# Kernel optimization log

Measured on AMD Instinct MI355X. Metric: run time of the kernel, lower is better.

The kernel has to match this reference:

```python
import jax, jax.numpy as jnp
import numpy as np


def setup_inputs() -> dict:
    key = jax.random.key(0)
    k1, k2, k3, k4 = jax.random.split(key, 4)
    B, N, F_in, F_out = 8, 2048, 256, 256
    v = jax.random.normal(k1, (B, N, F_in), dtype=jnp.float32)
    adj = jax.random.uniform(k2, (B, N, N), dtype=jnp.float32)  # pairwise distances
    # torch Linear weights: [out_features, in_features], scaled like kaiming-uniform-ish
    W1 = jax.random.normal(k3, (F_out, F_in), dtype=jnp.float32) * (1.0 / np.sqrt(F_in))
    W2 = jax.random.normal(k4, (F_out, F_in), dtype=jnp.float32) * (1.0 / np.sqrt(F_in))
    return {"v": v, "adj": adj, "W1": W1, "W2": W2}


def reference(v, adj, W1, W2):
    D = 100.0
    # Linear projections (no bias): [B,N,F_in] @ [F_in,F_out]
    c1 = jnp.einsum("bnf,of->bno", v, W1)
    c2 = jnp.einsum("bnf,of->bno", v, W2)
    # Pairwise scores: [B,N,N]
    s = jnp.einsum("bno,bmo->bnm", c1, c2)
    c = jax.nn.sigmoid(s) * D + 1e-05
    c = 1.0 / (2.0 * c * c)
    norm_adj = jnp.exp(-(adj * adj * c))
    return (v, norm_adj)
```

## Files before the change

### kernel.cpp

```cpp
#include <hip/hip_runtime.h>


typedef _Float16 half8_t __attribute__((ext_vector_type(8)));
typedef _Float16 half4_t __attribute__((ext_vector_type(4)));
typedef float floatx4 __attribute__((ext_vector_type(4)));

#define LDSS 72
#define PS   132

__global__ void prep_kernel(const floatx4* __restrict__ v4,
                            floatx4* __restrict__ out4,
                            half4_t* __restrict__ vf4) {
    int idx = blockIdx.x * 256 + threadIdx.x;
    floatx4 t = v4[idx];
    out4[idx] = t;
    half4_t h;
    h[0] = (_Float16)t[0]; h[1] = (_Float16)t[1];
    h[2] = (_Float16)t[2]; h[3] = (_Float16)t[3];
    vf4[idx] = h;
}

__global__ void mt_kernel(const float* __restrict__ W1,
                          const float* __restrict__ W2,
                          _Float16* __restrict__ Mt) {
    __shared__ float w2col[256];
    const int j = blockIdx.x;
    const int i = threadIdx.x;
    w2col[i] = W2[i * 256 + j];
    __syncthreads();
    float acc = 0.f;
    #pragma unroll 8
    for (int o = 0; o < 256; ++o)
        acc += w2col[o] * W1[o * 256 + i];
    Mt[j * 256 + i] = (_Float16)acc;
}

template<int MODE>
__global__ __launch_bounds__(256, 3)
void gemm_kernel(const _Float16* __restrict__ A, const _Float16* __restrict__ Bm,
                 size_t a_bstride, size_t b_bstride,
                 _Float16* __restrict__ Uout,
                 const float* __restrict__ adj, float* __restrict__ out) {
    __shared__ _Float16 smem[2 * 128 * LDSS];
    _Float16* As = smem;
    _Float16* Bs = smem + 128 * LDSS;

    const int tid  = threadIdx.x;
    const int lane = tid & 63;
    const int wid  = tid >> 6;
    const int wm   = wid >> 1;
    const int wn   = wid & 1;
    const int quad = lane >> 4;
    const int l16  = lane & 15;

    const int m0 = blockIdx.x * 128;
    const int n0 = blockIdx.y * 128;
    const int batch = blockIdx.z;

    const _Float16* Ab = A  + (size_t)batch * a_bstride;
    const _Float16* Bb = Bm + (size_t)batch * b_bstride;

    const int srow = tid >> 5;
    const int scol = (tid & 31) * 4;
    const size_t gbase = (size_t)batch * 2048 * 2048
                       + (size_t)m0 * 2048 + n0 + scol;

    floatx4 aj0[8];
    if (MODE == 1) {
        #pragma unroll
        for (int p = 0; p < 8; ++p)
            aj0[p] = __builtin_nontemporal_load(
                (const floatx4*)(adj + gbase + (size_t)(p * 8 + srow) * 2048));
        asm volatile("" ::: "memory");
    }

    floatx4 acc[4][4];
    #pragma unroll
    for (int i = 0; i < 4; ++i)
        #pragma unroll
        for (int j = 0; j < 4; ++j)
            acc[i][j] = (floatx4){0.f, 0.f, 0.f, 0.f};

    const int rrow = tid >> 3;
    const int ch8  = (tid & 7) * 8;

    #pragma unroll
    for (int kc = 0; kc < 256; kc += 64) {
        if (kc) __syncthreads();
        #pragma unroll
        for (int r = 0; r < 4; ++r) {
            int row = r * 32 + rrow;
            uint4 va = *(const uint4*)(Ab + (((size_t)(m0 + row)) << 8) + kc + ch8);
            uint4 vb = *(const uint4*)(Bb + (((size_t)(n0 + row)) << 8) + kc + ch8);
            *(uint4*)(&As[row * LDSS + ch8]) = va;
            *(uint4*)(&Bs[row * LDSS + ch8]) = vb;
        }
        __syncthreads();
        #pragma unroll
        for (int ks = 0; ks < 2; ++ks) {
            const int kof = ks * 32 + quad * 8;
            half8_t mf[4], nf[4];
            #pragma unroll
            for (int t = 0; t < 4; ++t) {
                mf[t] = *(const half8_t*)(&As[(wm * 64 + t * 16 + l16) * LDSS + kof]);
                nf[t] = *(const half8_t*)(&Bs[(wn * 64 + t * 16 + l16) * LDSS + kof]);
            }
            #pragma unroll
            for (int i = 0; i < 4; ++i)
                #pragma unroll
                for (int j = 0; j < 4; ++j)
                    acc[i][j] = __builtin_amdgcn_mfma_f32_16x16x32_f16(
                        nf[i], mf[j], acc[i][j], 0, 0, 0);
        }
    }

    if (MODE == 0) {
        #pragma unroll
        for (int j = 0; j < 4; ++j) {
            int m = m0 + wm * 64 + j * 16 + l16;
            #pragma unroll
            for (int i = 0; i < 4; ++i) {
                int n = wn * 64 + i * 16 + quad * 4;
                half4_t h;
                #pragma unroll
                for (int r = 0; r < 4; ++r) h[r] = (_Float16)acc[i][j][r];
                *(half4_t*)(Uout + (size_t)m * 256 + n0 + n) = h;
            }
        }
    } else {
        __syncthreads();
        _Float16* Ps = smem;
        #pragma unroll
        for (int j = 0; j < 4; ++j) {
            int ml = wm * 64 + j * 16 + l16;
            #pragma unroll
            for (int i = 0; i < 4; ++i) {
                int nl = wn * 64 + i * 16 + quad * 4;
                half4_t h;
                #pragma unroll
                for (int r = 0; r < 4; ++r) {
                    float s = acc[i][j][r];
                    float p = 100.0f / (1.0f + __expf(-s)) + 1e-5f;
                    h[r] = (_Float16)p;
                }
                *(half4_t*)(&Ps[ml * PS + nl]) = h;
            }
        }

        floatx4 aj1[8];
        #pragma unroll
        for (int p = 0; p < 8; ++p)
            aj1[p] = __builtin_nontemporal_load(
                (const floatx4*)(adj + gbase + (size_t)((p + 8) * 8 + srow) * 2048));
        asm volatile("" ::: "memory");

        __syncthreads();

        #pragma unroll
        for (int pass = 0; pass < 8; ++pass) {
            int r = pass * 8 + srow;
            size_t g = gbase + (size_t)r * 2048;
            floatx4 a = aj0[pass];
            half4_t ph = *(const half4_t*)(&Ps[r * PS + scol]);
            floatx4 o;
            #pragma unroll
            for (int e = 0; e < 4; ++e) {
                float ip = __builtin_amdgcn_rcpf((float)ph[e]);
                float q = a[e] * ip;
                o[e] = __expf(-0.5f * q * q);
            }
            __builtin_nontemporal_store(o, (floatx4*)(out + g));
        }
        #pragma unroll
        for (int pass = 8; pass < 16; ++pass) {
            int r = pass * 8 + srow;
            size_t g = gbase + (size_t)r * 2048;
            floatx4 a = aj1[pass - 8];
            half4_t ph = *(const half4_t*)(&Ps[r * PS + scol]);
            floatx4 o;
            #pragma unroll
            for (int e = 0; e < 4; ++e) {
                float ip = __builtin_amdgcn_rcpf((float)ph[e]);
                float q = a[e] * ip;
                o[e] = __expf(-0.5f * q * q);
            }
            __builtin_nontemporal_store(o, (floatx4*)(out + g));
        }
    }
}

extern "C" void kernel_launch(void* const* d_in, const int* in_sizes, int n_in,
                              void* d_out, int out_size, void* d_ws, size_t ws_size,
                              hipStream_t stream) {
    const float* v   = (const float*)d_in[0];
    const float* adj = (const float*)d_in[1];
    const float* W1  = (const float*)d_in[2];
    const float* W2  = (const float*)d_in[3];

    float* out_v   = (float*)d_out;
    float* out_adj = (float*)d_out + (size_t)8 * 2048 * 256;

    char* ws = (char*)d_ws;
    _Float16* vf = (_Float16*)ws;
    _Float16* uf = (_Float16*)(ws + ((size_t)8 << 20));
    _Float16* Mt = (_Float16*)(ws + ((size_t)16 << 20));

    prep_kernel<<<4096, 256, 0, stream>>>((const floatx4*)v, (floatx4*)out_v, (half4_t*)vf);
    mt_kernel<<<256, 256, 0, stream>>>(W1, W2, Mt);
    gemm_kernel<0><<<dim3(128, 2, 1), 256, 0, stream>>>(
        vf, Mt, 0, 0, uf, nullptr, nullptr);
    gemm_kernel<1><<<dim3(16, 16, 8), 256, 0, stream>>>(
        uf, vf, (size_t)2048 * 256, (size_t)2048 * 256, nullptr, adj, out_adj);
}
```

Baseline: 314.6 us.

## Make score-normalize GEMM persistent with cross-tile adjacency prefetch

```diff
diff --git a/kernel.cpp b/kernel.cpp
--- a/kernel.cpp
+++ b/kernel.cpp
@@ -52,69 +52,50 @@
     const int wn   = wid & 1;
     const int quad = lane >> 4;
     const int l16  = lane & 15;
-
-    const int m0 = blockIdx.x * 128;
-    const int n0 = blockIdx.y * 128;
-    const int batch = blockIdx.z;
-
-    const _Float16* Ab = A  + (size_t)batch * a_bstride;
-    const _Float16* Bb = Bm + (size_t)batch * b_bstride;
-
-    const int srow = tid >> 5;
-    const int scol = (tid & 31) * 4;
-    const size_t gbase = (size_t)batch * 2048 * 2048
-                       + (size_t)m0 * 2048 + n0 + scol;
-
-    floatx4 aj0[8];
-    if (MODE == 1) {
-        #pragma unroll
-        for (int p = 0; p < 8; ++p)
-            aj0[p] = __builtin_nontemporal_load(
-                (const floatx4*)(adj + gbase + (size_t)(p * 8 + srow) * 2048));
-        asm volatile("" ::: "memory");
-    }
-
-    floatx4 acc[4][4];
-    #pragma unroll
-    for (int i = 0; i < 4; ++i)
-        #pragma unroll
-        for (int j = 0; j < 4; ++j)
-            acc[i][j] = (floatx4){0.f, 0.f, 0.f, 0.f};
-
     const int rrow = tid >> 3;
     const int ch8  = (tid & 7) * 8;
 
-    #pragma unroll
-    for (int kc = 0; kc < 256; kc += 64) {
-        if (kc) __syncthreads();
-        #pragma unroll
-        for (int r = 0; r < 4; ++r) {
-            int row = r * 32 + rrow;
-            uint4 va = *(const uint4*)(Ab + (((size_t)(m0 + row)) << 8) + kc + ch8);
-            uint4 vb = *(const uint4*)(Bb + (((size_t)(n0 + row)) << 8) + kc + ch8);
-            *(uint4*)(&As[row * LDSS + ch8]) = va;
-            *(uint4*)(&Bs[row * LDSS + ch8]) = vb;
-        }
-        __syncthreads();
-        #pragma unroll
-        for (int ks = 0; ks < 2; ++ks) {
-            const int kof = ks * 32 + quad * 8;
-            half8_t mf[4], nf[4];
-            #pragma unroll
-            for (int t = 0; t < 4; ++t) {
-                mf[t] = *(const half8_t*)(&As[(wm * 64 + t * 16 + l16) * LDSS + kof]);
-                nf[t] = *(const half8_t*)(&Bs[(wn * 64 + t * 16 + l16) * LDSS + kof]);
-            }
-            #pragma unroll
-            for (int i = 0; i < 4; ++i)
-                #pragma unroll
-                for (int j = 0; j < 4; ++j)
-                    acc[i][j] = __builtin_amdgcn_mfma_f32_16x16x32_f16(
-                        nf[i], mf[j], acc[i][j], 0, 0, 0);
-        }
-    }
-
     if (MODE == 0) {
+        const int m0 = blockIdx.x * 128;
+        const int n0 = blockIdx.y * 128;
+
+        floatx4 acc[4][4];
+        #pragma unroll
+        for (int i = 0; i < 4; ++i)
+            #pragma unroll
+            for (int j = 0; j < 4; ++j)
+                acc[i][j] = (floatx4){0.f, 0.f, 0.f, 0.f};
+
+        #pragma unroll
+        for (int kc = 0; kc < 256; kc += 64) {
+            if (kc) __syncthreads();
+            #pragma unroll
+            for (int r = 0; r < 4; ++r) {
+                int row = r * 32 + rrow;
+                uint4 va = *(const uint4*)(A  + (((size_t)(m0 + row)) << 8) + kc + ch8);
+                uint4 vb = *(const uint4*)(Bm + (((size_t)(n0 + row)) << 8) + kc + ch8);
+                *(uint4*)(&As[row * LDSS + ch8]) = va;
+                *(uint4*)(&Bs[row * LDSS + ch8]) = vb;
+            }
+            __syncthreads();
+            #pragma unroll
+            for (int ks = 0; ks < 2; ++ks) {
+                const int kof = ks * 32 + quad * 8;
+                half8_t mf[4], nf[4];
+                #pragma unroll
+                for (int t = 0; t < 4; ++t) {
+                    mf[t] = *(const half8_t*)(&As[(wm * 64 + t * 16 + l16) * LDSS + kof]);
+                    nf[t] = *(const half8_t*)(&Bs[(wn * 64 + t * 16 + l16) * LDSS + kof]);
+                }
+                #pragma unroll
+                for (int i = 0; i < 4; ++i)
+                    #pragma unroll
+                    for (int j = 0; j < 4; ++j)
+                        acc[i][j] = __builtin_amdgcn_mfma_f32_16x16x32_f16(
+                            nf[i], mf[j], acc[i][j], 0, 0, 0);
+            }
+        }
+
         #pragma unroll
         for (int j = 0; j < 4; ++j) {
             int m = m0 + wm * 64 + j * 16 + l16;
@@ -127,7 +108,83 @@
                 *(half4_t*)(Uout + (size_t)m * 256 + n0 + n) = h;
             }
         }
-    } else {
+        return;
+    }
+
+    const int NT = 2048;
+    const int STRIDE = 768;
+
+    const int srow = tid >> 5;
+    const int scol = (tid & 31) * 4;
+
+    auto tile_gbase = [&](int t) -> size_t {
+        int batch = t >> 8;
+        int rem   = t & 255;
+        return (size_t)batch * 2048 * 2048
+             + (size_t)((rem >> 4) << 7) * 2048 + ((rem & 15) << 7) + scol;
+    };
+
+    int tile = blockIdx.x;
+
+    floatx4 aj0[8];
+    {
+        size_t g0 = tile_gbase(tile);
+        #pragma unroll
+        for (int p = 0; p < 8; ++p)
+            aj0[p] = __builtin_nontemporal_load(
+                (const floatx4*)(adj + g0 + (size_t)(p * 8 + srow) * 2048));
+        asm volatile("" ::: "memory");
+    }
+
+    bool first = true;
+    for (; tile < NT; tile += STRIDE) {
+        const int batch = tile >> 8;
+        const int rem   = tile & 255;
+        const int m0    = (rem >> 4) << 7;
+        const int n0    = (rem & 15) << 7;
+        const _Float16* Ab = A  + (size_t)batch * a_bstride;
+        const _Float16* Bb = Bm + (size_t)batch * b_bstride;
+        const size_t gbase = (size_t)batch * 2048 * 2048
+                           + (size_t)m0 * 2048 + n0 + scol;
+
+        floatx4 acc[4][4];
+        #pragma unroll
+        for (int i = 0; i < 4; ++i)
+            #pragma unroll
+            for (int j = 0; j < 4; ++j)
+                acc[i][j] = (floatx4){0.f, 0.f, 0.f, 0.f};
+
+        #pragma unroll
+        for (int kc = 0; kc < 256; kc += 64) {
+            if (!first || kc) __syncthreads();
+            #pragma unroll
+            for (int r = 0; r < 4; ++r) {
+                int row = r * 32 + rrow;
+                uint4 va = *(const uint4*)(Ab + (((size_t)(m0 + row)) << 8) + kc + ch8);
+                uint4 vb = *(const uint4*)(Bb + (((size_t)(n0 + row)) << 8) + kc + ch8);
+                *(uint4*)(&As[row * LDSS + ch8]) = va;
+                *(uint4*)(&Bs[row * LDSS + ch8]) = vb;
+            }
+            __syncthreads();
+            #pragma unroll
+            for (int ks = 0; ks < 2; ++ks) {
+                const int kof = ks * 32 + quad * 8;
+                half8_t mf[4], nf[4];
+                #pragma unroll
+                for (int t = 0; t < 4; ++t) {
+                    mf[t] = *(const half8_t*)(&As[(wm * 64 + t * 16 + l16) * LDSS + kof]);
+                    nf[t] = *(const half8_t*)(&Bs[(wn * 64 + t * 16 + l16) * LDSS + kof]);
+                }
+                #pragma unroll
+                for (int i = 0; i < 4; ++i)
+                    #pragma unroll
+                    for (int j = 0; j < 4; ++j)
+                        acc[i][j] = __builtin_amdgcn_mfma_f32_16x16x32_f16(
+                            nf[i], mf[j], acc[i][j], 0, 0, 0);
+            }
+        }
+        first = false;
+
         __syncthreads();
         _Float16* Ps = smem;
         #pragma unroll
@@ -156,6 +213,10 @@
 
         __syncthreads();
 
+        const int  ntile   = tile + STRIDE;
+        const bool hasnext = ntile < NT;
+        const size_t ngbase = hasnext ? tile_gbase(ntile) : 0;
+
         #pragma unroll
         for (int pass = 0; pass < 8; ++pass) {
             int r = pass * 8 + srow;
@@ -170,7 +231,12 @@
                 o[e] = __expf(-0.5f * q * q);
             }
             __builtin_nontemporal_store(o, (floatx4*)(out + g));
-        }
+            if (hasnext)
+                aj0[pass] = __builtin_nontemporal_load(
+                    (const floatx4*)(adj + ngbase + (size_t)r * 2048));
+        }
+        asm volatile("" ::: "memory");
+
         #pragma unroll
         for (int pass = 8; pass < 16; ++pass) {
             int r = pass * 8 + srow;
@@ -209,6 +275,6 @@
     mt_kernel<<<256, 256, 0, stream>>>(W1, W2, Mt);
     gemm_kernel<0><<<dim3(128, 2, 1), 256, 0, stream>>>(
         vf, Mt, 0, 0, uf, nullptr, nullptr);
-    gemm_kernel<1><<<dim3(16, 16, 8), 256, 0, stream>>>(
+    gemm_kernel<1><<<dim3(768, 1, 1), 256, 0, stream>>>(
         uf, vf, (size_t)2048 * 256, (size_t)2048 * 256, nullptr, adj, out_adj);
 }
```

Measured after the change: 333.6 us. +6.1%, slower.
